# Performance work log

Measured on AMD Instinct MI355X. Metric: run time of the kernel, lower is better.

The kernel has to match this reference:

```python
import jax, jax.numpy as jnp
import numpy as np

B, Q, V, H = 32, 1, 4096, 1024


def setup_inputs() -> dict:
    key = jax.random.key(0)
    ks = jax.random.split(key, 8)
    query = jax.random.normal(ks[0], (B, Q, H), dtype=jnp.float32)
    key_t = jax.random.normal(ks[1], (B, V, H), dtype=jnp.float32)
    value = jax.random.normal(ks[2], (B, V, H), dtype=jnp.float32)
    # nn.Linear weights stored as (out, in); bias init U(-0.1, 0.1)
    scale = 1.0 / np.sqrt(H)
    Wq = jax.random.uniform(ks[3], (H, H), minval=-scale, maxval=scale, dtype=jnp.float32)
    Wk = jax.random.uniform(ks[4], (H, H), minval=-scale, maxval=scale, dtype=jnp.float32)
    bias = jax.random.uniform(ks[5], (H,), minval=-0.1, maxval=0.1, dtype=jnp.float32)
    Ws = jax.random.uniform(ks[6], (1, H), minval=-scale, maxval=scale, dtype=jnp.float32)
    bs = jax.random.uniform(ks[7], (1,), minval=-scale, maxval=scale, dtype=jnp.float32)
    return {"query": query, "key": key_t, "value": value,
            "Wq": Wq, "Wk": Wk, "bias": bias, "Ws": Ws, "bs": bs}


def reference(query, key, value, Wq, Wk, bias, Ws, bs):
    # score_proj(tanh(key_proj(key) + query_proj(query) + bias)).squeeze(-1)
    kp = jnp.einsum('bvh,oh->bvo', key, Wk)            # (B, V, H)
    qp = jnp.einsum('bqh,oh->bqo', query, Wq)          # (B, 1, H)
    h = jnp.tanh(kp + qp + bias)                       # (B, V, H)
    score = jnp.einsum('bvh,oh->bvo', h, Ws)[..., 0] + bs[0]  # (B, V)
    attn = jax.nn.softmax(score, axis=-1)              # (B, V)
    context = jnp.einsum('bv,bvh->bh', attn, value)[:, None, :]  # (B, 1, H)
    return context, attn
```

## Files before the change

kernel.cpp:

```cpp
#include <hip/hip_runtime.h>
#include <stdint.h>

#define B_ 32
#define V_ 4096
#define H_ 1024

typedef __bf16 bf16x8 __attribute__((ext_vector_type(8)));
typedef float f32x4 __attribute__((ext_vector_type(4)));

__device__ __forceinline__ unsigned short f2bf(float x) {
    unsigned int u = __float_as_uint(x);
    u += 0x7fffu + ((u >> 16) & 1u);
    return (unsigned short)(u >> 16);
}

__global__ __launch_bounds__(256) void wk_to_bf16(const float* __restrict__ wk,
                                                  unsigned short* __restrict__ out) {
    int i = (blockIdx.x * 256 + threadIdx.x) * 4;
    float4 f = *(const float4*)(wk + i);
    ushort4 u;
    u.x = f2bf(f.x); u.y = f2bf(f.y); u.z = f2bf(f.z); u.w = f2bf(f.w);
    *(ushort4*)(out + i) = u;
}

__global__ __launch_bounds__(256) void compute_r(const float* __restrict__ query,
                                                 const float* __restrict__ wq,
                                                 const float* __restrict__ bias,
                                                 float* __restrict__ r) {
    int gid = blockIdx.x * 4 + (threadIdx.x >> 6);
    int lane = threadIdx.x & 63;
    int b = gid & 31;
    int o = gid >> 5;
    const float4* q4 = (const float4*)(query + b * H_);
    const float4* w4 = (const float4*)(wq + (size_t)o * H_);
    float s = 0.f;
    #pragma unroll
    for (int i = 0; i < 4; ++i) {
        float4 q = q4[lane + i * 64];
        float4 w = w4[lane + i * 64];
        s += q.x * w.x + q.y * w.y + q.z * w.z + q.w * w.w;
    }
    #pragma unroll
    for (int m = 32; m >= 1; m >>= 1) s += __shfl_xor(s, m, 64);
    if (lane == 0) r[b * H_ + o] = s + bias[o];
}

__global__ __launch_bounds__(512) void score_kernel(const float* __restrict__ key,
                                                    const unsigned short* __restrict__ wkb,
                                                    const float* __restrict__ r,
                                                    const float* __restrict__ wsc,
                                                    float* __restrict__ score) {
    __shared__ unsigned short Alds[64 * 1032];
    __shared__ unsigned short Blds[256 * 40];
    __shared__ float scoreLds[64];

    int t = threadIdx.x;
    int b = blockIdx.x >> 6;
    int v0 = (blockIdx.x & 63) << 6;
    int lane = t & 63;
    int wid = t >> 6;
    int waveM = wid >> 2;
    int waveN = wid & 3;
    int l15 = lane & 15;
    int l4 = lane >> 4;

    {
        const float* kbase = key + ((size_t)(b * V_ + v0)) * H_;
        int row = t >> 3;
        int j = t & 7;
        const float4* src = (const float4*)(kbase + (size_t)row * H_);
        unsigned short* dst = Alds + row * 1032;
        #pragma unroll
        for (int it = 0; it < 32; ++it) {
            int c4 = j + it * 8;
            float4 f = src[c4];
            ushort4 u;
            u.x = f2bf(f.x); u.y = f2bf(f.y); u.z = f2bf(f.z); u.w = f2bf(f.w);
            *(ushort4*)(dst + c4 * 4) = u;
        }
    }
    if (t < 64) scoreLds[t] = 0.f;

    int o_stage = t >> 1;
    int kh = t & 1;

    for (int ot = 0; ot < 4; ++ot) {
        int obase = ot * 256;
        f32x4 acc[2][4];
        #pragma unroll
        for (int mi = 0; mi < 2; ++mi)
            #pragma unroll
            for (int nj = 0; nj < 4; ++nj)
                acc[mi][nj] = (f32x4){0.f, 0.f, 0.f, 0.f};

        for (int kc = 0; kc < 32; ++kc) {
            const uint4* gsrc = (const uint4*)(wkb + (size_t)(obase + o_stage) * H_ + kc * 32 + kh * 16);
            uint4 g0 = gsrc[0];
            uint4 g1 = gsrc[1];
            __syncthreads();
            uint4* bdst = (uint4*)(Blds + o_stage * 40 + kh * 16);
            bdst[0] = g0; bdst[1] = g1;
            __syncthreads();

            bf16x8 af[2];
            #pragma unroll
            for (int mi = 0; mi < 2; ++mi)
                af[mi] = *(const bf16x8*)(Alds + (waveM * 32 + mi * 16 + l15) * 1032 + kc * 32 + l4 * 8);
            #pragma unroll
            for (int nj = 0; nj < 4; ++nj) {
                bf16x8 bf = *(const bf16x8*)(Blds + (waveN * 64 + nj * 16 + l15) * 40 + l4 * 8);
                acc[0][nj] = __builtin_amdgcn_mfma_f32_16x16x32_bf16(af[0], bf, acc[0][nj], 0, 0, 0);
                acc[1][nj] = __builtin_amdgcn_mfma_f32_16x16x32_bf16(af[1], bf, acc[1][nj], 0, 0, 0);
            }
        }

        float rv[4], wv[4];
        #pragma unroll
        for (int nj = 0; nj < 4; ++nj) {
            int o = obase + waveN * 64 + nj * 16 + l15;
            rv[nj] = r[b * H_ + o];
            wv[nj] = wsc[o];
        }
        #pragma unroll
        for (int mi = 0; mi < 2; ++mi) {
            #pragma unroll
            for (int reg = 0; reg < 4; ++reg) {
                float s = 0.f;
                #pragma unroll
                for (int nj = 0; nj < 4; ++nj) {
                    float x = acc[mi][nj][reg] + rv[nj];
                    float e = __expf(2.f * x);
                    float th = 1.f - 2.f / (e + 1.f);
                    s += th * wv[nj];
                }
                #pragma unroll
                for (int m = 1; m < 16; m <<= 1) s += __shfl_xor(s, m, 64);
                if (l15 == 0) {
                    int vl = waveM * 32 + mi * 16 + l4 * 4 + reg;
                    atomicAdd(&scoreLds[vl], s);
                }
            }
        }
    }
    __syncthreads();
    if (t < 64) score[b * V_ + v0 + t] = scoreLds[t];
}

__global__ __launch_bounds__(256) void softmax_kernel(const float* __restrict__ score,
                                                      float* __restrict__ attn) {
    int b = blockIdx.x, t = threadIdx.x;
    __shared__ float red[8];
    const float* s = score + b * V_;
    float v[16];
    float mx = -1e30f;
    #pragma unroll
    for (int i = 0; i < 16; ++i) { v[i] = s[t + i * 256]; mx = fmaxf(mx, v[i]); }
    #pragma unroll
    for (int m = 32; m >= 1; m >>= 1) mx = fmaxf(mx, __shfl_xor(mx, m, 64));
    if ((t & 63) == 0) red[t >> 6] = mx;
    __syncthreads();
    mx = fmaxf(fmaxf(red[0], red[1]), fmaxf(red[2], red[3]));
    float sum = 0.f;
    #pragma unroll
    for (int i = 0; i < 16; ++i) { v[i] = __expf(v[i] - mx); sum += v[i]; }
    #pragma unroll
    for (int m = 32; m >= 1; m >>= 1) sum += __shfl_xor(sum, m, 64);
    if ((t & 63) == 0) red[4 + (t >> 6)] = sum;
    __syncthreads();
    float inv = 1.f / (red[4] + red[5] + red[6] + red[7]);
    float* a = attn + b * V_;
    #pragma unroll
    for (int i = 0; i < 16; ++i) a[t + i * 256] = v[i] * inv;
}

__global__ __launch_bounds__(256) void context_kernel(const float* __restrict__ value,
                                                      const float* __restrict__ attn,
                                                      float* __restrict__ ctx) {
    int b = blockIdx.x, hc = blockIdx.y, vc = blockIdx.z, t = threadIdx.x;
    __shared__ float a[512];
    int vb = vc * 512;
    a[t] = attn[b * V_ + vb + t];
    a[t + 256] = attn[b * V_ + vb + t + 256];
    __syncthreads();
    int h = hc * 256 + t;
    const float* vp = value + ((size_t)(b * V_ + vb)) * H_ + h;
    float acc = 0.f;
    #pragma unroll 8
    for (int i = 0; i < 512; ++i) acc += a[i] * vp[(size_t)i * H_];
    atomicAdd(&ctx[b * H_ + h], acc);
}

extern "C" void kernel_launch(void* const* d_in, const int* in_sizes, int n_in,
                              void* d_out, int out_size, void* d_ws, size_t ws_size,
                              hipStream_t stream) {
    const float* query = (const float*)d_in[0];
    const float* key   = (const float*)d_in[1];
    const float* value = (const float*)d_in[2];
    const float* Wq    = (const float*)d_in[3];
    const float* Wk    = (const float*)d_in[4];
    const float* bias  = (const float*)d_in[5];
    const float* Wsv   = (const float*)d_in[6];

    unsigned short* wkb = (unsigned short*)d_ws;
    float* r     = (float*)((char*)d_ws + (2u << 20));
    float* score = (float*)((char*)d_ws + (2u << 20) + (128u << 10));

    float* ctx  = (float*)d_out;
    float* attn = (float*)d_out + 32 * 1024;

    hipMemsetAsync(ctx, 0, 32 * 1024 * sizeof(float), stream);
    wk_to_bf16<<<1024, 256, 0, stream>>>(Wk, wkb);
    compute_r<<<8192, 256, 0, stream>>>(query, Wq, bias, r);
    score_kernel<<<2048, 512, 0, stream>>>(key, wkb, r, Wsv, score);
    softmax_kernel<<<32, 256, 0, stream>>>(score, attn);
    context_kernel<<<dim3(32, 4, 8), 256, 0, stream>>>(value, attn, ctx);
}
```

Baseline: 1.622 ms.

## Software-pipeline Wk tile loads and XOR-swizzle key tile in score kernel

Restructures the score kernel's main loop to double-buffer the Wk global loads in registers, prefetching the next k-slice while the current one is written to LDS and consumed, using raw s_barrier with explicit waitcnt. The key tile in LDS drops its padding in favor of an XOR swizzle and is loaded with 8-wide converts. The per-o-tile shuffle reductions and LDS atomics are deferred into register accumulators and done once at the end. This is meant to hide global-load latency and cut per-tile reduction overhead, at the cost of hand-managed barriers that are easy to get wrong.

```diff
diff --git a/kernel.cpp b/kernel.cpp
--- a/kernel.cpp
+++ b/kernel.cpp
@@ -7,6 +7,7 @@
 
 typedef __bf16 bf16x8 __attribute__((ext_vector_type(8)));
 typedef float f32x4 __attribute__((ext_vector_type(4)));
+typedef unsigned short u16x8 __attribute__((ext_vector_type(8)));
 
 __device__ __forceinline__ unsigned short f2bf(float x) {
     unsigned int u = __float_as_uint(x);
@@ -50,9 +51,8 @@
                                                     const float* __restrict__ r,
                                                     const float* __restrict__ wsc,
                                                     float* __restrict__ score) {
-    __shared__ unsigned short Alds[64 * 1032];
+    __shared__ unsigned short Alds[64 * 1024];
     __shared__ unsigned short Blds[256 * 40];
-    __shared__ float scoreLds[64];
 
     int t = threadIdx.x;
     int b = blockIdx.x >> 6;
@@ -64,56 +64,53 @@
     int l15 = lane & 15;
     int l4 = lane >> 4;
 
+    int o_r = t >> 1;
+    int kh = t & 1;
+    const unsigned short* wsrc = wkb + (size_t)o_r * H_ + kh * 16;
+    unsigned short* bdst = Blds + o_r * 40 + kh * 16;
+
+    uint4 g0a = *(const uint4*)(wsrc);
+    uint4 g0b = *(const uint4*)(wsrc + 8);
+    uint4 g1a = *(const uint4*)(wsrc + 32);
+    uint4 g1b = *(const uint4*)(wsrc + 40);
+
     {
-        const float* kbase = key + ((size_t)(b * V_ + v0)) * H_;
         int row = t >> 3;
         int j = t & 7;
-        const float4* src = (const float4*)(kbase + (size_t)row * H_);
-        unsigned short* dst = Alds + row * 1032;
-        #pragma unroll
-        for (int it = 0; it < 32; ++it) {
-            int c4 = j + it * 8;
-            float4 f = src[c4];
-            ushort4 u;
-            u.x = f2bf(f.x); u.y = f2bf(f.y); u.z = f2bf(f.z); u.w = f2bf(f.w);
-            *(ushort4*)(dst + c4 * 4) = u;
+        const float4* src = (const float4*)(key + ((size_t)(b * V_ + v0) + row) * H_);
+        unsigned short* dst = Alds + row * 1024;
+        int swz = (row & 15) << 3;
+        #pragma unroll 8
+        for (int it = 0; it < 16; ++it) {
+            int c = j + it * 8;
+            float4 f0 = src[2 * c];
+            float4 f1 = src[2 * c + 1];
+            u16x8 u;
+            u[0] = f2bf(f0.x); u[1] = f2bf(f0.y); u[2] = f2bf(f0.z); u[3] = f2bf(f0.w);
+            u[4] = f2bf(f1.x); u[5] = f2bf(f1.y); u[6] = f2bf(f1.z); u[7] = f2bf(f1.w);
+            *(u16x8*)(dst + ((c * 8) ^ swz)) = u;
         }
     }
-    if (t < 64) scoreLds[t] = 0.f;
-
-    int o_stage = t >> 1;
-    int kh = t & 1;
+
+    const unsigned short* aBase0 = Alds + (waveM * 32 + l15) * 1024;
+    const unsigned short* aBase1 = aBase0 + 16 * 1024;
+    const unsigned short* bBase = Blds + (waveN * 64 + l15) * 40 + l4 * 8;
+    int aswz = l15 << 3;
+
+    float sAcc[2][4];
+    #pragma unroll
+    for (int mi = 0; mi < 2; ++mi)
+        #pragma unroll
+        for (int rg = 0; rg < 4; ++rg) sAcc[mi][rg] = 0.f;
 
     for (int ot = 0; ot < 4; ++ot) {
-        int obase = ot * 256;
+        int obase = ot << 8;
         f32x4 acc[2][4];
         #pragma unroll
         for (int mi = 0; mi < 2; ++mi)
             #pragma unroll
             for (int nj = 0; nj < 4; ++nj)
                 acc[mi][nj] = (f32x4){0.f, 0.f, 0.f, 0.f};
-
-        for (int kc = 0; kc < 32; ++kc) {
-            const uint4* gsrc = (const uint4*)(wkb + (size_t)(obase + o_stage) * H_ + kc * 32 + kh * 16);
-            uint4 g0 = gsrc[0];
-            uint4 g1 = gsrc[1];
-            __syncthreads();
-            uint4* bdst = (uint4*)(Blds + o_stage * 40 + kh * 16);
-            bdst[0] = g0; bdst[1] = g1;
-            __syncthreads();
-
-            bf16x8 af[2];
-            #pragma unroll
-            for (int mi = 0; mi < 2; ++mi)
-                af[mi] = *(const bf16x8*)(Alds + (waveM * 32 + mi * 16 + l15) * 1032 + kc * 32 + l4 * 8);
-            #pragma unroll
-            for (int nj = 0; nj < 4; ++nj) {
-                bf16x8 bf = *(const bf16x8*)(Blds + (waveN * 64 + nj * 16 + l15) * 40 + l4 * 8);
-                acc[0][nj] = __builtin_amdgcn_mfma_f32_16x16x32_bf16(af[0], bf, acc[0][nj], 0, 0, 0);
-                acc[1][nj] = __builtin_amdgcn_mfma_f32_16x16x32_bf16(af[1], bf, acc[1][nj], 0, 0, 0);
-            }
-        }
-
         float rv[4], wv[4];
         #pragma unroll
         for (int nj = 0; nj < 4; ++nj) {
@@ -121,29 +118,91 @@
             rv[nj] = r[b * H_ + o];
             wv[nj] = wsc[o];
         }
-        #pragma unroll
-        for (int mi = 0; mi < 2; ++mi) {
+
+        for (int kc = 0; kc < 32; kc += 2) {
+            __builtin_amdgcn_s_barrier();
+            asm volatile("" ::: "memory");
+            *(uint4*)(bdst) = g0a;
+            *(uint4*)(bdst + 8) = g0b;
+            {
+                int fs = ot * 32 + kc + 2;
+                const unsigned short* p = wsrc + (fs >> 5) * (256 * H_) + (fs & 31) * 32;
+                g0a = *(const uint4*)(p);
+                g0b = *(const uint4*)(p + 8);
+            }
+            asm volatile("s_waitcnt lgkmcnt(0)" ::: "memory");
+            __builtin_amdgcn_s_barrier();
+            asm volatile("" ::: "memory");
+            {
+                int aoff = (kc * 32 + l4 * 8) ^ aswz;
+                bf16x8 af0 = *(const bf16x8*)(aBase0 + aoff);
+                bf16x8 af1 = *(const bf16x8*)(aBase1 + aoff);
+                #pragma unroll
+                for (int nj = 0; nj < 4; ++nj) {
+                    bf16x8 bv = *(const bf16x8*)(bBase + nj * (16 * 40));
+                    acc[0][nj] = __builtin_amdgcn_mfma_f32_16x16x32_bf16(af0, bv, acc[0][nj], 0, 0, 0);
+                    acc[1][nj] = __builtin_amdgcn_mfma_f32_16x16x32_bf16(af1, bv, acc[1][nj], 0, 0, 0);
+                }
+            }
+            __builtin_amdgcn_s_barrier();
+            asm volatile("" ::: "memory");
+            *(uint4*)(bdst) = g1a;
+            *(uint4*)(bdst + 8) = g1b;
+            {
+                int fs = ot * 32 + kc + 3;
+                const unsigned short* p = wsrc + (fs >> 5) * (256 * H_) + (fs & 31) * 32;
+                g1a = *(const uint4*)(p);
+                g1b = *(const uint4*)(p + 8);
+            }
+            asm volatile("s_waitcnt lgkmcnt(0)" ::: "memory");
+            __builtin_amdgcn_s_barrier();
+            asm volatile("" ::: "memory");
+            {
+                int aoff = ((kc + 1) * 32 + l4 * 8) ^ aswz;
+                bf16x8 af0 = *(const bf16x8*)(aBase0 + aoff);
+                bf16x8 af1 = *(const bf16x8*)(aBase1 + aoff);
+                #pragma unroll
+                for (int nj = 0; nj < 4; ++nj) {
+                    bf16x8 bv = *(const bf16x8*)(bBase + nj * (16 * 40));
+                    acc[0][nj] = __builtin_amdgcn_mfma_f32_16x16x32_bf16(af0, bv, acc[0][nj], 0, 0, 0);
+                    acc[1][nj] = __builtin_amdgcn_mfma_f32_16x16x32_bf16(af1, bv, acc[1][nj], 0, 0, 0);
+                }
+            }
+        }
+
+        #pragma unroll
+        for (int mi = 0; mi < 2; ++mi)
             #pragma unroll
-            for (int reg = 0; reg < 4; ++reg) {
+            for (int rg = 0; rg < 4; ++rg) {
                 float s = 0.f;
                 #pragma unroll
                 for (int nj = 0; nj < 4; ++nj) {
-                    float x = acc[mi][nj][reg] + rv[nj];
+                    float x = acc[mi][nj][rg] + rv[nj];
                     float e = __expf(2.f * x);
                     float th = 1.f - 2.f / (e + 1.f);
                     s += th * wv[nj];
                 }
-                #pragma unroll
-                for (int m = 1; m < 16; m <<= 1) s += __shfl_xor(s, m, 64);
-                if (l15 == 0) {
-                    int vl = waveM * 32 + mi * 16 + l4 * 4 + reg;
-                    atomicAdd(&scoreLds[vl], s);
-                }
-            }
-        }
+                sAcc[mi][rg] += s;
+            }
     }
-    __syncthreads();
-    if (t < 64) score[b * V_ + v0 + t] = scoreLds[t];
+
+    __syncthreads();
+    float* sb = (float*)Alds;
+    if (t < 64) sb[t] = 0.f;
+    __syncthreads();
+    #pragma unroll
+    for (int mi = 0; mi < 2; ++mi)
+        #pragma unroll
+        for (int rg = 0; rg < 4; ++rg) {
+            float s = sAcc[mi][rg];
+            s += __shfl_xor(s, 1, 64);
+            s += __shfl_xor(s, 2, 64);
+            s += __shfl_xor(s, 4, 64);
+            s += __shfl_xor(s, 8, 64);
+            if (l15 == 0) atomicAdd(&sb[waveM * 32 + mi * 16 + l4 * 4 + rg], s);
+        }
+    __syncthreads();
+    if (t < 64) score[b * V_ + v0 + t] = sb[t];
 }
 
 __global__ __launch_bounds__(256) void softmax_kernel(const float* __restrict__ score,
```

Result: faster. 1.386 ms (-14.6%).
